# Performance work log

Hardware: AMD Instinct MI355X
Metric: run time of the kernel (lower is better)

The kernel has to match this reference:

```python
import jax, jax.numpy as jnp
import numpy as np

B, S, E, H = 2, 2048, 1024, 16
HD = E // H            # head_dim = 64
ROT = 64               # rotary_dim == head_dim
BASE = 10000.0


def setup_inputs() -> dict:
    key = jax.random.key(0)
    k1, k2, k3, k4, k5 = jax.random.split(key, 5)
    return {
        "x": jax.random.normal(k1, (B, S, E), dtype=jnp.float32),
        "mask": jnp.ones((B, S), dtype=jnp.int32),
        "qkv_w": jax.random.normal(k2, (3 * E, E), dtype=jnp.float32) * (1.0 / np.sqrt(E)),
        "qkv_b": jax.random.normal(k3, (3 * E,), dtype=jnp.float32) * 0.02,
        "out_w": jax.random.normal(k4, (E, E), dtype=jnp.float32) * (1.0 / np.sqrt(E)),
        "out_b": jax.random.normal(k5, (E,), dtype=jnp.float32) * 0.02,
    }


def _rotate_half(x):
    # split last dim into (even, odd) pairs and rotate 90 degrees
    x = x.reshape(*x.shape[:-1], -1, 2)
    x1, x2 = x[..., 0], x[..., 1]
    return jnp.stack((-x2, x1), axis=-1).reshape(*x.shape[:-2], -1)


def _rope_cos_sin(seq_len, rot_dim, dtype):
    inv_freq = 1.0 / (BASE ** (jnp.arange(0, rot_dim, 2, dtype=jnp.float32) / rot_dim))
    freqs = jnp.arange(seq_len, dtype=jnp.float32)[:, None] * inv_freq[None, :]  # [S, rot/2]
    cos = jnp.repeat(jnp.cos(freqs), 2, axis=-1).astype(dtype)  # [S, rot]
    sin = jnp.repeat(jnp.sin(freqs), 2, axis=-1).astype(dtype)
    return cos, sin


def reference(x, mask, qkv_w, qkv_b, out_w, out_b):
    b, s, _ = x.shape
    qkv = x @ qkv_w.T + qkv_b                      # [B,S,3E]
    q, k, v = jnp.split(qkv, 3, axis=-1)
    shape = lambda t: t.reshape(b, s, H, HD).transpose(0, 2, 1, 3)  # [B,H,S,HD]
    q, k, v = shape(q), shape(k), shape(v)

    cos, sin = _rope_cos_sin(s, ROT, q.dtype)      # [S, ROT]
    cos = cos[None, None]                          # [1,1,S,ROT]
    sin = sin[None, None]
    q_rot, q_pass = q[..., :ROT], q[..., ROT:]
    k_rot, k_pass = k[..., :ROT], k[..., ROT:]
    q = jnp.concatenate((q_rot * cos + _rotate_half(q_rot) * sin, q_pass), axis=-1)
    k = jnp.concatenate((k_rot * cos + _rotate_half(k_rot) * sin, k_pass), axis=-1)

    scale = 1.0 / np.sqrt(HD)
    scores = jnp.einsum("bhqd,bhkd->bhqk", q, k) * scale  # [B,H,S,S]
    keep = (mask != 0)[:, None, None, :]           # [B,1,1,S]
    scores = jnp.where(keep, scores, -jnp.inf)
    attn = jax.nn.softmax(scores, axis=-1)
    context = jnp.einsum("bhqk,bhkd->bhqd", attn, v)
    context = context.transpose(0, 2, 1, 3).reshape(b, s, E)
    return context @ out_w.T + out_b
```

## Files before the change

### kernel.cpp

```cpp
#include <hip/hip_runtime.h>
#include <hip/hip_bf16.h>
#include <cmath>

#define SB 2048
#define EB 1024
#define NH 16
#define HD 64
#define KLOG 0.14391156831212788f

typedef unsigned short u16;
typedef unsigned int u32;
typedef __attribute__((ext_vector_type(8))) short short8;
typedef __attribute__((ext_vector_type(4))) float f32x4;

__device__ __forceinline__ u16 f2b(float x) {
  __hip_bfloat16 h = __float2bfloat16(x);
  return *reinterpret_cast<u16*>(&h);
}

__device__ __forceinline__ void gl_lds16(const u16* g, u16* l) {
  __builtin_amdgcn_global_load_lds(
      (const __attribute__((address_space(1))) unsigned int*)g,
      (__attribute__((address_space(3))) unsigned int*)l, 16, 0, 0);
}

#define CN1 (4096 * 1024 / 4)
#define CN2 (3072 * 1024 / 4)
#define CN3 (1024 * 1024 / 4)
__global__ __launch_bounds__(256) void conv_all(
    const float* __restrict__ x, const float* __restrict__ w1,
    const float* __restrict__ w2, u16* __restrict__ xb,
    u16* __restrict__ wqb, u16* __restrict__ owb) {
  int i = blockIdx.x * 256 + threadIdx.x;
  const float* src;
  u16* dst;
  int j;
  if (i < CN1) { src = x; dst = xb; j = i; }
  else if (i < CN1 + CN2) { src = w1; dst = wqb; j = i - CN1; }
  else if (i < CN1 + CN2 + CN3) { src = w2; dst = owb; j = i - CN1 - CN2; }
  else return;
  float4 v = ((const float4*)src)[j];
  ushort4 o;
  o.x = f2b(v.x); o.y = f2b(v.y); o.z = f2b(v.z); o.w = f2b(v.w);
  ((ushort4*)dst)[j] = o;
}

__global__ __launch_bounds__(256) void qkv_mfma_rope(
    const u16* __restrict__ A, const u16* __restrict__ Bw,
    const float* __restrict__ bias, u16* __restrict__ qb,
    u16* __restrict__ kb, u16* __restrict__ vt) {
  __shared__ u16 As[128 * 32];
  __shared__ u16 Bs[128 * 32];
  __shared__ float CS[128 * 32];
  __shared__ float SN[128 * 32];

  const int t = threadIdx.x;
  const int lane = t & 63, wv = t >> 6;
  const int l15 = lane & 15, quad = lane >> 4;
  const int wm = wv >> 1, wn = wv & 1;
  const int m0 = blockIdx.x * 128;
  const int n0 = blockIdx.y * 128;

  f32x4 acc[4][4] = {};

  for (int k0 = 0; k0 < 1024; k0 += 32) {
#pragma unroll
    for (int c = 0; c < 2; c++) {
      int r = wv * 32 + c * 16;
      const u16* ga = A + (size_t)(m0 + r + (lane >> 2)) * 1024 + k0 + (lane & 3) * 8;
      const u16* gb = Bw + (size_t)(n0 + r + (lane >> 2)) * 1024 + k0 + (lane & 3) * 8;
      gl_lds16(ga, &As[r * 32]);
      gl_lds16(gb, &Bs[r * 32]);
    }
    __syncthreads();

    short8 a[4], b[4];
#pragma unroll
    for (int mi = 0; mi < 4; mi++)
      a[mi] = *(const short8*)&As[(wm * 64 + mi * 16 + l15) * 32 + quad * 8];
#pragma unroll
    for (int ni = 0; ni < 4; ni++)
      b[ni] = *(const short8*)&Bs[(wn * 64 + ni * 16 + l15) * 32 + quad * 8];
#pragma unroll
    for (int mi = 0; mi < 4; mi++)
#pragma unroll
      for (int ni = 0; ni < 4; ni++)
        acc[mi][ni] = __builtin_amdgcn_mfma_f32_16x16x32_bf16(a[mi], b[ni], acc[mi][ni], 0, 0, 0);
    __syncthreads();
  }

  const int n_base = n0 + wn * 64;
  const int which = n_base >> 10;
  float b4[4];
#pragma unroll
  for (int ni = 0; ni < 4; ni++) b4[ni] = bias[n_base + ni * 16 + l15];

  if (which < 2) {
#pragma unroll
    for (int i = 0; i < 16; i++) {
      int idx = t + i * 256;
      int row = idx >> 5, p = idx & 31;
      float spos = (float)((m0 & 2047) + row);
      float theta = spos * expf(-(float)(2 * p) * KLOG);
      float sn_, cs_;
      sincosf(theta, &sn_, &cs_);
      CS[idx] = cs_; SN[idx] = sn_;
    }
    __syncthreads();
  }

  const int h = (n_base & 1023) >> 6;
#pragma unroll
  for (int mi = 0; mi < 4; mi++) {
#pragma unroll
    for (int r = 0; r < 4; r++) {
      int row = wm * 64 + mi * 16 + quad * 4 + r;
      int m = m0 + row;
      int bb = m >> 11, s = m & 2047;
      if (which < 2) {
        u16* dst = (which == 0) ? qb : kb;
        size_t obase = ((size_t)(bb * NH + h) * SB + s) * HD;
#pragma unroll
        for (int ni = 0; ni < 4; ni++) {
          float v = acc[mi][ni][r] + b4[ni];
          int d = ni * 16 + l15;
          float pv = __shfl_xor(v, 1, 64);
          float c = CS[row * 32 + (d >> 1)];
          float sn_ = SN[row * 32 + (d >> 1)];
          v = v * c + pv * ((d & 1) ? sn_ : -sn_);
          if (which == 0) v *= 0.125f;
          dst[obase + d] = f2b(v);
        }
      } else {
        size_t tbase = (size_t)(bb * NH + h) * HD;
#pragma unroll
        for (int ni = 0; ni < 4; ni++) {
          float v = acc[mi][ni][r] + b4[ni];
          int d = ni * 16 + l15;
          vt[(tbase + d) * SB + s] = f2b(v);
        }
      }
    }
  }
}

__global__ __launch_bounds__(256) void attn_mfma(
    const u16* __restrict__ qb, const u16* __restrict__ kb,
    const u16* __restrict__ vt, const int* __restrict__ mask,
    u16* __restrict__ ctx) {
  __shared__ u16 Ks[64][72];
  __shared__ u16 Vt[64][72];
  __shared__ u32 Ps2[4][32][20];
  __shared__ int mks[64];

  const int bh = blockIdx.x, b = bh >> 4, h = bh & 15;
  const int q0 = blockIdx.y * 128;
  const int t = threadIdx.x;
  const int lane = t & 63, wv = t >> 6;
  const int l15 = lane & 15, quad = lane >> 4;

  short8 bq[2][2];
#pragma unroll
  for (int qh = 0; qh < 2; qh++) {
    const u16* qp = qb + ((size_t)bh * SB + q0 + wv * 32 + qh * 16 + l15) * HD;
#pragma unroll
    for (int kk = 0; kk < 2; kk++)
      bq[qh][kk] = *(const short8*)&qp[kk * 32 + quad * 8];
  }

  f32x4 o[2][4] = {};
  float m_i[2] = {-INFINITY, -INFINITY};
  float l_i[2] = {0.f, 0.f};

  for (int kt = 0; kt < SB / 64; kt++) {
    __syncthreads();
#pragma unroll
    for (int i = 0; i < 2; i++) {
      int idx = t + i * 256;
      int r = idx >> 3, c = idx & 7;
      *(uint4*)&Ks[r][c * 8] =
          *(const uint4*)&kb[((size_t)bh * SB + kt * 64 + r) * HD + c * 8];
      *(uint4*)&Vt[r][c * 8] =
          *(const uint4*)&vt[((size_t)bh * HD + r) * SB + kt * 64 + c * 8];
    }
    if (t < 64) mks[t] = mask[b * SB + kt * 64 + t];
    __syncthreads();

    short8 ak[4][2], av[4][2];
    int mk4[4][4];
#pragma unroll
    for (int mb = 0; mb < 4; mb++) {
#pragma unroll
      for (int kk = 0; kk < 2; kk++) {
        ak[mb][kk] = *(const short8*)&Ks[mb * 16 + l15][kk * 32 + quad * 8];
        av[mb][kk] = *(const short8*)&Vt[mb * 16 + l15][kk * 32 + quad * 8];
      }
      int4 mv = *(const int4*)&mks[mb * 16 + quad * 4];
      mk4[mb][0] = mv.x; mk4[mb][1] = mv.y; mk4[mb][2] = mv.z; mk4[mb][3] = mv.w;
    }

#pragma unroll
    for (int qh = 0; qh < 2; qh++) {
      f32x4 s[4] = {};
#pragma unroll
      for (int mb = 0; mb < 4; mb++) {
        s[mb] = __builtin_amdgcn_mfma_f32_16x16x32_bf16(ak[mb][0], bq[qh][0], s[mb], 0, 0, 0);
        s[mb] = __builtin_amdgcn_mfma_f32_16x16x32_bf16(ak[mb][1], bq[qh][1], s[mb], 0, 0, 0);
      }
      float mx = -INFINITY;
#pragma unroll
      for (int mb = 0; mb < 4; mb++)
#pragma unroll
        for (int r = 0; r < 4; r++) {
          float sv = mk4[mb][r] ? s[mb][r] : -INFINITY;
          s[mb][r] = sv;
          mx = fmaxf(mx, sv);
        }
      mx = fmaxf(mx, __shfl_xor(mx, 16, 64));
      mx = fmaxf(mx, __shfl_xor(mx, 32, 64));
      float mn = fmaxf(m_i[qh], mx);
      float mn_s = (mn == -INFINITY) ? 0.f : mn;
      float a = __expf(m_i[qh] - mn_s);
      float rs = 0.f;
#pragma unroll
      for (int mb = 0; mb < 4; mb++)
#pragma unroll
        for (int r = 0; r < 4; r++) {
          float p = __expf(s[mb][r] - mn_s);
          s[mb][r] = p;
          rs += p;
        }
      rs += __shfl_xor(rs, 16, 64);
      rs += __shfl_xor(rs, 32, 64);
      l_i[qh] = l_i[qh] * a + rs;
      m_i[qh] = mn;

#pragma unroll
      for (int mb = 0; mb < 4; mb++)
#pragma unroll
        for (int pr = 0; pr < 2; pr++) {
          u32 pk = (u32)f2b(s[mb][2 * pr]) | ((u32)f2b(s[mb][2 * pr + 1]) << 16);
          Ps2[wv][mb * 8 + quad * 2 + pr][l15] = pk;
        }
      short8 pb[2];
#pragma unroll
      for (int kk = 0; kk < 2; kk++) {
        u32 w[4];
#pragma unroll
        for (int j = 0; j < 4; j++)
          w[j] = Ps2[wv][kk * 16 + quad * 4 + j][l15];
        pb[kk] = *(const short8*)w;
      }
#pragma unroll
      for (int nb = 0; nb < 4; nb++) {
#pragma unroll
        for (int r = 0; r < 4; r++) o[qh][nb][r] *= a;
        o[qh][nb] = __builtin_amdgcn_mfma_f32_16x16x32_bf16(av[nb][0], pb[0], o[qh][nb], 0, 0, 0);
        o[qh][nb] = __builtin_amdgcn_mfma_f32_16x16x32_bf16(av[nb][1], pb[1], o[qh][nb], 0, 0, 0);
      }
    }
  }

#pragma unroll
  for (int qh = 0; qh < 2; qh++) {
    float linv = 1.f / l_i[qh];
    int qrow = q0 + wv * 32 + qh * 16 + l15;
    size_t base = ((size_t)b * SB + qrow) * EB + h * HD;
#pragma unroll
    for (int nb = 0; nb < 4; nb++)
#pragma unroll
      for (int pr = 0; pr < 2; pr++) {
        int d = nb * 16 + quad * 4 + 2 * pr;
        u32 pk = (u32)f2b(o[qh][nb][2 * pr] * linv) |
                 ((u32)f2b(o[qh][nb][2 * pr + 1] * linv) << 16);
        *(u32*)&ctx[base + d] = pk;
      }
  }
}

__global__ __launch_bounds__(256) void out_mfma(
    const u16* __restrict__ A, const u16* __restrict__ Bw,
    const float* __restrict__ bias, float* __restrict__ out) {
  __shared__ u16 As[128 * 32];
  __shared__ u16 Bs[128 * 32];

  const int t = threadIdx.x;
  const int lane = t & 63, wv = t >> 6;
  const int l15 = lane & 15, quad = lane >> 4;
  const int wm = wv >> 1, wn = wv & 1;
  const int m0 = blockIdx.x * 128;
  const int n0 = blockIdx.y * 128;

  f32x4 acc[4][4] = {};

  for (int k0 = 0; k0 < 1024; k0 += 32) {
#pragma unroll
    for (int c = 0; c < 2; c++) {
      int r = wv * 32 + c * 16;
      const u16* ga = A + (size_t)(m0 + r + (lane >> 2)) * 1024 + k0 + (lane & 3) * 8;
      const u16* gb = Bw + (size_t)(n0 + r + (lane >> 2)) * 1024 + k0 + (lane & 3) * 8;
      gl_lds16(ga, &As[r * 32]);
      gl_lds16(gb, &Bs[r * 32]);
    }
    __syncthreads();

    short8 a[4], b[4];
#pragma unroll
    for (int mi = 0; mi < 4; mi++)
      a[mi] = *(const short8*)&As[(wm * 64 + mi * 16 + l15) * 32 + quad * 8];
#pragma unroll
    for (int ni = 0; ni < 4; ni++)
      b[ni] = *(const short8*)&Bs[(wn * 64 + ni * 16 + l15) * 32 + quad * 8];
#pragma unroll
    for (int mi = 0; mi < 4; mi++)
#pragma unroll
      for (int ni = 0; ni < 4; ni++)
        acc[mi][ni] = __builtin_amdgcn_mfma_f32_16x16x32_bf16(a[mi], b[ni], acc[mi][ni], 0, 0, 0);
    __syncthreads();
  }

  float b4[4];
#pragma unroll
  for (int ni = 0; ni < 4; ni++) b4[ni] = bias[n0 + wn * 64 + ni * 16 + l15];
#pragma unroll
  for (int mi = 0; mi < 4; mi++)
#pragma unroll
    for (int r = 0; r < 4; r++) {
      int m = m0 + wm * 64 + mi * 16 + quad * 4 + r;
#pragma unroll
      for (int ni = 0; ni < 4; ni++)
        out[(size_t)m * 1024 + n0 + wn * 64 + ni * 16 + l15] = acc[mi][ni][r] + b4[ni];
    }
}

extern "C" void kernel_launch(void* const* d_in, const int* in_sizes, int n_in,
                              void* d_out, int out_size, void* d_ws, size_t ws_size,
                              hipStream_t stream) {
  const float* x     = (const float*)d_in[0];
  const int* mask    = (const int*)d_in[1];
  const float* qkv_w = (const float*)d_in[2];
  const float* qkv_b = (const float*)d_in[3];
  const float* out_w = (const float*)d_in[4];
  const float* out_b = (const float*)d_in[5];
  float* out = (float*)d_out;

  char* wsb = (char*)d_ws;
  u16* xb  = (u16*)wsb;
  u16* wqb = (u16*)(wsb + ( 8ull << 20));
  u16* owb = (u16*)(wsb + (14ull << 20));
  u16* qb  = (u16*)(wsb + (16ull << 20));
  u16* kb  = (u16*)(wsb + (24ull << 20));
  u16* vtb = (u16*)(wsb + (32ull << 20));
  u16* cxb = (u16*)(wsb + (40ull << 20));

  dim3 blk(256);
  hipLaunchKernelGGL(conv_all, dim3((CN1 + CN2 + CN3 + 255) / 256), blk, 0, stream,
                     x, qkv_w, out_w, xb, wqb, owb);

  hipLaunchKernelGGL(qkv_mfma_rope, dim3(32, 24), blk, 0, stream,
                     xb, wqb, qkv_b, qb, kb, vtb);

  hipLaunchKernelGGL(attn_mfma, dim3(32, 16), blk, 0, stream, qb, kb, vtb, mask, cxb);

  hipLaunchKernelGGL(out_mfma, dim3(32, 8), blk, 0, stream, cxb, owb, out_b, out);
}
```

Before: 226.2 us.

## Halve attention query tile and register-prefetch next K/V tile

The attention kernel now gives each block 64 query rows (16 per wave) instead of 128, which doubles the grid to 1024 blocks. It also prefetches the next K, V and mask tile into registers while the current tile is processed. K and V fragments are read from LDS just before each MFMA instead of being held in registers, which lowers register pressure. The aim is more occupancy and latency hiding, at the cost of loading each K/V tile twice as often from global memory/L2.

```diff
diff --git a/kernel.cpp b/kernel.cpp
--- a/kernel.cpp
+++ b/kernel.cpp
@@ -154,125 +154,132 @@
   __shared__ int mks[64];
 
   const int bh = blockIdx.x, b = bh >> 4, h = bh & 15;
-  const int q0 = blockIdx.y * 128;
+  const int q0 = blockIdx.y * 64;
   const int t = threadIdx.x;
   const int lane = t & 63, wv = t >> 6;
   const int l15 = lane & 15, quad = lane >> 4;
 
-  short8 bq[2][2];
-#pragma unroll
-  for (int qh = 0; qh < 2; qh++) {
-    const u16* qp = qb + ((size_t)bh * SB + q0 + wv * 32 + qh * 16 + l15) * HD;
-#pragma unroll
-    for (int kk = 0; kk < 2; kk++)
-      bq[qh][kk] = *(const short8*)&qp[kk * 32 + quad * 8];
-  }
-
-  f32x4 o[2][4] = {};
-  float m_i[2] = {-INFINITY, -INFINITY};
-  float l_i[2] = {0.f, 0.f};
+  short8 bq[2];
+  {
+    const u16* qp = qb + ((size_t)bh * SB + q0 + wv * 16 + l15) * HD;
+    bq[0] = *(const short8*)&qp[quad * 8];
+    bq[1] = *(const short8*)&qp[32 + quad * 8];
+  }
+
+  f32x4 o[4] = {};
+  float m_i = -INFINITY, l_i = 0.f;
+
+  const int sr = t >> 3, sc = t & 7;
+  uint4 kreg[2], vreg[2];
+  int mreg = 0;
+#pragma unroll
+  for (int i = 0; i < 2; i++) {
+    int r = sr + i * 32;
+    kreg[i] = *(const uint4*)&kb[((size_t)bh * SB + r) * HD + sc * 8];
+    vreg[i] = *(const uint4*)&vt[((size_t)bh * HD + r) * SB + sc * 8];
+  }
+  if (t < 64) mreg = mask[b * SB + t];
 
   for (int kt = 0; kt < SB / 64; kt++) {
     __syncthreads();
 #pragma unroll
     for (int i = 0; i < 2; i++) {
-      int idx = t + i * 256;
-      int r = idx >> 3, c = idx & 7;
-      *(uint4*)&Ks[r][c * 8] =
-          *(const uint4*)&kb[((size_t)bh * SB + kt * 64 + r) * HD + c * 8];
-      *(uint4*)&Vt[r][c * 8] =
-          *(const uint4*)&vt[((size_t)bh * HD + r) * SB + kt * 64 + c * 8];
-    }
-    if (t < 64) mks[t] = mask[b * SB + kt * 64 + t];
-    __syncthreads();
-
-    short8 ak[4][2], av[4][2];
-    int mk4[4][4];
+      int r = sr + i * 32;
+      *(uint4*)&Ks[r][sc * 8] = kreg[i];
+      *(uint4*)&Vt[r][sc * 8] = vreg[i];
+    }
+    if (t < 64) mks[t] = mreg;
+    {
+      int ktn = (kt + 1 < SB / 64) ? kt + 1 : kt;
+#pragma unroll
+      for (int i = 0; i < 2; i++) {
+        int r = sr + i * 32;
+        kreg[i] = *(const uint4*)&kb[((size_t)bh * SB + ktn * 64 + r) * HD + sc * 8];
+        vreg[i] = *(const uint4*)&vt[((size_t)bh * HD + r) * SB + ktn * 64 + sc * 8];
+      }
+      if (t < 64) mreg = mask[b * SB + ktn * 64 + t];
+    }
+    __syncthreads();
+
+    f32x4 s[4] = {};
 #pragma unroll
     for (int mb = 0; mb < 4; mb++) {
-#pragma unroll
-      for (int kk = 0; kk < 2; kk++) {
-        ak[mb][kk] = *(const short8*)&Ks[mb * 16 + l15][kk * 32 + quad * 8];
-        av[mb][kk] = *(const short8*)&Vt[mb * 16 + l15][kk * 32 + quad * 8];
-      }
+      short8 a0 = *(const short8*)&Ks[mb * 16 + l15][quad * 8];
+      short8 a1 = *(const short8*)&Ks[mb * 16 + l15][32 + quad * 8];
+      s[mb] = __builtin_amdgcn_mfma_f32_16x16x32_bf16(a0, bq[0], s[mb], 0, 0, 0);
+      s[mb] = __builtin_amdgcn_mfma_f32_16x16x32_bf16(a1, bq[1], s[mb], 0, 0, 0);
+    }
+
+    float mx = -INFINITY;
+#pragma unroll
+    for (int mb = 0; mb < 4; mb++) {
       int4 mv = *(const int4*)&mks[mb * 16 + quad * 4];
-      mk4[mb][0] = mv.x; mk4[mb][1] = mv.y; mk4[mb][2] = mv.z; mk4[mb][3] = mv.w;
-    }
-
-#pragma unroll
-    for (int qh = 0; qh < 2; qh++) {
-      f32x4 s[4] = {};
-#pragma unroll
-      for (int mb = 0; mb < 4; mb++) {
-        s[mb] = __builtin_amdgcn_mfma_f32_16x16x32_bf16(ak[mb][0], bq[qh][0], s[mb], 0, 0, 0);
-        s[mb] = __builtin_amdgcn_mfma_f32_16x16x32_bf16(ak[mb][1], bq[qh][1], s[mb], 0, 0, 0);
-      }
-      float mx = -INFINITY;
-#pragma unroll
-      for (int mb = 0; mb < 4; mb++)
-#pragma unroll
-        for (int r = 0; r < 4; r++) {
-          float sv = mk4[mb][r] ? s[mb][r] : -INFINITY;
-          s[mb][r] = sv;
-          mx = fmaxf(mx, sv);
-        }
-      mx = fmaxf(mx, __shfl_xor(mx, 16, 64));
-      mx = fmaxf(mx, __shfl_xor(mx, 32, 64));
-      float mn = fmaxf(m_i[qh], mx);
-      float mn_s = (mn == -INFINITY) ? 0.f : mn;
-      float a = __expf(m_i[qh] - mn_s);
-      float rs = 0.f;
-#pragma unroll
-      for (int mb = 0; mb < 4; mb++)
-#pragma unroll
-        for (int r = 0; r < 4; r++) {
-          float p = __expf(s[mb][r] - mn_s);
-          s[mb][r] = p;
-          rs += p;
-        }
-      rs += __shfl_xor(rs, 16, 64);
-      rs += __shfl_xor(rs, 32, 64);
-      l_i[qh] = l_i[qh] * a + rs;
-      m_i[qh] = mn;
-
-#pragma unroll
-      for (int mb = 0; mb < 4; mb++)
-#pragma unroll
-        for (int pr = 0; pr < 2; pr++) {
-          u32 pk = (u32)f2b(s[mb][2 * pr]) | ((u32)f2b(s[mb][2 * pr + 1]) << 16);
-          Ps2[wv][mb * 8 + quad * 2 + pr][l15] = pk;
-        }
-      short8 pb[2];
-#pragma unroll
-      for (int kk = 0; kk < 2; kk++) {
-        u32 w[4];
-#pragma unroll
-        for (int j = 0; j < 4; j++)
-          w[j] = Ps2[wv][kk * 16 + quad * 4 + j][l15];
-        pb[kk] = *(const short8*)w;
-      }
-#pragma unroll
-      for (int nb = 0; nb < 4; nb++) {
-#pragma unroll
-        for (int r = 0; r < 4; r++) o[qh][nb][r] *= a;
-        o[qh][nb] = __builtin_amdgcn_mfma_f32_16x16x32_bf16(av[nb][0], pb[0], o[qh][nb], 0, 0, 0);
-        o[qh][nb] = __builtin_amdgcn_mfma_f32_16x16x32_bf16(av[nb][1], pb[1], o[qh][nb], 0, 0, 0);
-      }
-    }
-  }
-
-#pragma unroll
-  for (int qh = 0; qh < 2; qh++) {
-    float linv = 1.f / l_i[qh];
-    int qrow = q0 + wv * 32 + qh * 16 + l15;
+      int mk4[4] = {mv.x, mv.y, mv.z, mv.w};
+#pragma unroll
+      for (int r = 0; r < 4; r++) {
+        float sv = mk4[r] ? s[mb][r] : -INFINITY;
+        s[mb][r] = sv;
+        mx = fmaxf(mx, sv);
+      }
+    }
+    mx = fmaxf(mx, __shfl_xor(mx, 16, 64));
+    mx = fmaxf(mx, __shfl_xor(mx, 32, 64));
+    float mn = fmaxf(m_i, mx);
+    float mn_s = (mn == -INFINITY) ? 0.f : mn;
+    float a = __expf(m_i - mn_s);
+    float rs = 0.f;
+#pragma unroll
+    for (int mb = 0; mb < 4; mb++)
+#pragma unroll
+      for (int r = 0; r < 4; r++) {
+        float p = __expf(s[mb][r] - mn_s);
+        s[mb][r] = p;
+        rs += p;
+      }
+    rs += __shfl_xor(rs, 16, 64);
+    rs += __shfl_xor(rs, 32, 64);
+    l_i = l_i * a + rs;
+    m_i = mn;
+
+#pragma unroll
+    for (int mb = 0; mb < 4; mb++)
+#pragma unroll
+      for (int pr = 0; pr < 2; pr++) {
+        u32 pk = (u32)f2b(s[mb][2 * pr]) | ((u32)f2b(s[mb][2 * pr + 1]) << 16);
+        Ps2[wv][mb * 8 + quad * 2 + pr][l15] = pk;
+      }
+    short8 pb[2];
+#pragma unroll
+    for (int kk = 0; kk < 2; kk++) {
+      u32 w[4];
+#pragma unroll
+      for (int j = 0; j < 4; j++)
+        w[j] = Ps2[wv][kk * 16 + quad * 4 + j][l15];
+      pb[kk] = *(const short8*)w;
+    }
+
+#pragma unroll
+    for (int nb = 0; nb < 4; nb++) {
+      short8 v0 = *(const short8*)&Vt[nb * 16 + l15][quad * 8];
+      short8 v1 = *(const short8*)&Vt[nb * 16 + l15][32 + quad * 8];
+#pragma unroll
+      for (int r = 0; r < 4; r++) o[nb][r] *= a;
+      o[nb] = __builtin_amdgcn_mfma_f32_16x16x32_bf16(v0, pb[0], o[nb], 0, 0, 0);
+      o[nb] = __builtin_amdgcn_mfma_f32_16x16x32_bf16(v1, pb[1], o[nb], 0, 0, 0);
+    }
+  }
+
+  {
+    float linv = 1.f / l_i;
+    int qrow = q0 + wv * 16 + l15;
     size_t base = ((size_t)b * SB + qrow) * EB + h * HD;
 #pragma unroll
     for (int nb = 0; nb < 4; nb++)
 #pragma unroll
       for (int pr = 0; pr < 2; pr++) {
         int d = nb * 16 + quad * 4 + 2 * pr;
-        u32 pk = (u32)f2b(o[qh][nb][2 * pr] * linv) |
-                 ((u32)f2b(o[qh][nb][2 * pr + 1] * linv) << 16);
+        u32 pk = (u32)f2b(o[nb][2 * pr] * linv) |
+                 ((u32)f2b(o[nb][2 * pr + 1] * linv) << 16);
         *(u32*)&ctx[base + d] = pk;
       }
   }
@@ -360,7 +367,7 @@
   hipLaunchKernelGGL(qkv_mfma_rope, dim3(32, 24), blk, 0, stream,
                      xb, wqb, qkv_b, qb, kb, vtb);
 
-  hipLaunchKernelGGL(attn_mfma, dim3(32, 16), blk, 0, stream, qb, kb, vtb, mask, cxb);
+  hipLaunchKernelGGL(attn_mfma, dim3(32, 32), blk, 0, stream, qb, kb, vtb, mask, cxb);
 
   hipLaunchKernelGGL(out_mfma, dim3(32, 8), blk, 0, stream, cxb, owb, out_b, out);
 }
```

After: 299.2 us. 32.2% more time.
